# Kernel tuning notes

Hardware: AMD Instinct MI355X
Metric: run time of the kernel (lower is better)

## Reference

```python
import jax, jax.numpy as jnp
import numpy as np

NC, NX, NY = 32, 512, 512
N_LOC = 100000


def setup_inputs() -> dict:
    key = jax.random.key(0)
    k1, k2 = jax.random.split(key)
    x = jax.random.normal(k1, (8, NC, NX, NY), dtype=jnp.float32)
    kernel = jnp.zeros((1, NC, NX, NY), dtype=jnp.float32)
    variable_kernel = jax.random.normal(k2, (N_LOC,), dtype=jnp.float32)
    # unique flat indices into the (NC, NX, NY) kernel volume (cluster locations)
    rng = np.random.default_rng(0)
    loc_idx = jnp.asarray(rng.choice(NC * NX * NY, N_LOC, replace=False).astype(np.int64))
    return {"x": x, "kernel": kernel, "variable_kernel": variable_kernel, "loc_idx": loc_idx}


def fill_kernel(kernel, variable_kernel, loc_idx):
    # scatter ReLU'd trainable values into the sparse PSF locations
    k0 = kernel[0].reshape(-1).at[loc_idx].set(jax.nn.relu(variable_kernel))
    return k0.reshape(NC, NX, NY)


def disperse_all_orders(x, k):
    # per-channel circular convolution with the multi-order dispersion PSF,
    # summed over spectral channels onto the sensor: (b, nx, ny)
    Xf = jnp.fft.rfft2(x, axes=(-2, -1))          # (b, nc, nx, ny//2+1)
    Kf = jnp.fft.rfft2(k, axes=(-2, -1))          # (nc, nx, ny//2+1)
    Yf = jnp.sum(Xf * Kf[None], axis=1)           # (b, nx, ny//2+1)
    return jnp.fft.irfft2(Yf, s=(NX, NY), axes=(-2, -1))


def reference(x, kernel, variable_kernel, loc_idx):
    k = fill_kernel(kernel, variable_kernel, loc_idx)
    return disperse_all_orders(x, k)
```

## Files before the change

kernel.cpp:

```cpp
#include <hip/hip_runtime.h>
#include <cstdint>

#define NXX 512
#define NYY 512
#define NCH 32
#define NB  8
#define NU  257
#define IMG_CPLX (NU*NXX)
#define PIX (NXX*NYY)

__device__ __forceinline__ uint32_t f2bf(float f){
  uint32_t u = __float_as_uint(f);
  return (u + 0x7FFFu + ((u >> 16) & 1u)) >> 16;
}
__device__ __forceinline__ float bf2f(uint32_t h){ return __uint_as_float(h << 16); }
__device__ __forceinline__ uint32_t packbf(float re, float im){ return f2bf(re) | (f2bf(im) << 16); }

#define WAIT_LGKM() asm volatile("s_waitcnt lgkmcnt(0)" ::: "memory")

__device__ __forceinline__ void cmul(float& zr, float& zi, float wr, float wi){
  float r = zr*wr - zi*wi;
  zi = zr*wi + zi*wr;
  zr = r;
}

template<int DIR>
__device__ __forceinline__ void bfly8(float* xr, float* xi){
  const float S = 0.70710678118654752440f;
  float er0=xr[0]+xr[4], ei0=xi[0]+xi[4];
  float er1=xr[1]+xr[5], ei1=xi[1]+xi[5];
  float er2=xr[2]+xr[6], ei2=xi[2]+xi[6];
  float er3=xr[3]+xr[7], ei3=xi[3]+xi[7];
  float or0=xr[0]-xr[4], oi0=xi[0]-xi[4];
  float or1=xr[1]-xr[5], oi1=xi[1]-xi[5];
  float or2=xr[2]-xr[6], oi2=xi[2]-xi[6];
  float or3=xr[3]-xr[7], oi3=xi[3]-xi[7];
  float p0r=er0+er2, p0i=ei0+ei2;
  float p1r=er0-er2, p1i=ei0-ei2;
  float q0r=er1+er3, q0i=ei1+ei3;
  float q1r=er1-er3, q1i=ei1-ei3;
  float w4r, w4i;
  if (DIR<0){ w4r=q1i; w4i=-q1r; } else { w4r=-q1i; w4i=q1r; }
  xr[0]=p0r+q0r; xi[0]=p0i+q0i;
  xr[4]=p0r-q0r; xi[4]=p0i-q0i;
  xr[2]=p1r+w4r; xi[2]=p1i+w4i;
  xr[6]=p1r-w4r; xi[6]=p1i-w4i;
  float f1r,f1i,f2r,f2i,f3r,f3i;
  if (DIR<0){
    f1r=S*(or1+oi1); f1i=S*(oi1-or1);
    f2r=oi2;         f2i=-or2;
    f3r=S*(oi3-or3); f3i=-S*(or3+oi3);
  } else {
    f1r=S*(or1-oi1);  f1i=S*(or1+oi1);
    f2r=-oi2;         f2i=or2;
    f3r=-S*(or3+oi3); f3i=S*(or3-oi3);
  }
  float g0r=or0+f2r, g0i=oi0+f2i;
  float g1r=or0-f2r, g1i=oi0-f2i;
  float h0r=f1r+f3r, h0i=f1i+f3i;
  float h1r=f1r-f3r, h1i=f1i-f3i;
  float v4r, v4i;
  if (DIR<0){ v4r=h1i; v4i=-h1r; } else { v4r=-h1i; v4i=h1r; }
  xr[1]=g0r+h0r; xi[1]=g0i+h0i;
  xr[5]=g0r-h0r; xi[5]=g0i-h0i;
  xr[3]=g1r+v4r; xi[3]=g1i+v4i;
  xr[7]=g1r-v4r; xi[7]=g1i-v4i;
}

__device__ __forceinline__ void make_tw(int t, float* t1r, float* t1i, float* t2r, float* t2i){
  const float TP = 6.283185307179586476925f;
  float s, c;
  sincosf(-TP * (float)t * (1.0f/512.0f), &s, &c);
  t1r[0]=1.0f; t1i[0]=0.0f;
  #pragma unroll
  for (int k=1;k<8;k++){ t1r[k]=t1r[k-1]*c - t1i[k-1]*s; t1i[k]=t1r[k-1]*s + t1i[k-1]*c; }
  sincosf(-TP * (float)(t>>3) * (1.0f/64.0f), &s, &c);
  t2r[0]=1.0f; t2i[0]=0.0f;
  #pragma unroll
  for (int k=1;k<8;k++){ t2r[k]=t2r[k-1]*c - t2i[k-1]*s; t2i[k]=t2r[k-1]*s + t2i[k-1]*c; }
}

template<int DIR>
__device__ __forceinline__ void fft512(float* ar, float* ai, float* sre, float* sim, int t,
    const float* t1r, const float* t1i, const float* t2r, const float* t2i){
  bfly8<DIR>(ar, ai);
  #pragma unroll
  for (int k=1;k<8;k++){ cmul(ar[k], ai[k], t1r[k], (DIR<0)? t1i[k] : -t1i[k]); }
  #pragma unroll
  for (int k=0;k<8;k++){ int d = 8*t + k; d += (d>>5); sre[d]=ar[k]; sim[d]=ai[k]; }
  WAIT_LGKM();
  #pragma unroll
  for (int j=0;j<8;j++){ int s2 = t + (j<<6); s2 += (s2>>5); ar[j]=sre[s2]; ai[j]=sim[s2]; }
  WAIT_LGKM();
  bfly8<DIR>(ar, ai);
  #pragma unroll
  for (int k=1;k<8;k++){ cmul(ar[k], ai[k], t2r[k], (DIR<0)? t2i[k] : -t2i[k]); }
  #pragma unroll
  for (int k=0;k<8;k++){ int d = (t&7) + ((t>>3)<<6) + (k<<3); d += (d>>5); sre[d]=ar[k]; sim[d]=ai[k]; }
  WAIT_LGKM();
  #pragma unroll
  for (int j=0;j<8;j++){ int s2 = t + (j<<6); s2 += (s2>>5); ar[j]=sre[s2]; ai[j]=sim[s2]; }
  WAIT_LGKM();
  bfly8<DIR>(ar, ai);
}

__global__ __launch_bounds__(256) void k_zero(uint4* __restrict__ p, int n4){
  int stride = gridDim.x * 256;
  for (int i = blockIdx.x*256 + threadIdx.x; i < n4; i += stride)
    p[i] = make_uint4(0u,0u,0u,0u);
}

__global__ void k_scatter(const float* __restrict__ vk, const int* __restrict__ loc,
                          float* __restrict__ kbuf, int n){
  int i = blockIdx.x*256 + threadIdx.x;
  if (i < n){ float v = vk[i]; kbuf[loc[i]] = v > 0.0f ? v : 0.0f; }
}

__global__ __launch_bounds__(512) void k_p1(const float* __restrict__ src,
                                            uint32_t* __restrict__ dst){
  __shared__ float sre[8][528], sim[8][528];
  __shared__ uint32_t staged[NU*33];
  const int tid = threadIdx.x;
  const int w = tid >> 6, t = tid & 63;
  const int img = blockIdx.x >> 4;
  const int rblock = (blockIdx.x & 15) << 5;
  float t1r[8],t1i[8],t2r[8],t2i[8];
  make_tw(t, t1r,t1i,t2r,t2i);
  #pragma unroll
  for (int p=0; p<2; p++){
    const int il = (w<<2) + (p<<1);
    const float* rowA = src + (size_t)img*PIX + (size_t)(rblock + il)*NYY;
    float ar[8], ai[8];
    #pragma unroll
    for (int j=0;j<8;j++){ ar[j]=rowA[t+(j<<6)]; ai[j]=rowA[NYY + t + (j<<6)]; }
    fft512<-1>(ar,ai,sre[w],sim[w],t,t1r,t1i,t2r,t2i);
    #pragma unroll
    for (int k=0;k<8;k++){ int d = t+(k<<6); d += (d>>5); sre[w][d]=ar[k]; sim[w][d]=ai[k]; }
    WAIT_LGKM();
    #pragma unroll
    for (int k=0;k<5;k++){
      int u = t + (k<<6);
      if (u < NU){
        int e2 = (512 - u) & 511;
        int du = u + (u>>5), d2 = e2 + (e2>>5);
        float zur=sre[w][du], zui=sim[w][du];
        float zvr=sre[w][d2], zvi=sim[w][d2];
        float Ar=0.5f*(zur+zvr), Ai=0.5f*(zui-zvi);
        float Br=0.5f*(zui+zvi), Bi=0.5f*(zvr-zur);
        staged[u*33 + il]     = packbf(Ar,Ai);
        staged[u*33 + il + 1] = packbf(Br,Bi);
      }
    }
    WAIT_LGKM();
  }
  __syncthreads();
  uint32_t* ob = dst + (size_t)img*IMG_CPLX;
  for (int e = tid; e < NU*32; e += 512){
    int u = e >> 5, il2 = e & 31;
    ob[(size_t)u*NXX + rblock + il2] = staged[u*33 + il2];
  }
}

__global__ __launch_bounds__(512) void k_p2k(uint32_t* __restrict__ rtk){
  __shared__ float sre[8][528], sim[8][528];
  const int w = threadIdx.x >> 6, t = threadIdx.x & 63;
  const int fid = blockIdx.x*8 + w;
  const int c = fid / NU, u = fid % NU;
  float t1r[8],t1i[8],t2r[8],t2i[8];
  make_tw(t, t1r,t1i,t2r,t2i);
  uint32_t* col = rtk + (size_t)c*IMG_CPLX + (size_t)u*NXX;
  float ar[8], ai[8];
  #pragma unroll
  for (int j=0;j<8;j++){ uint32_t v = col[t+(j<<6)]; ar[j]=bf2f(v & 0xFFFFu); ai[j]=bf2f(v >> 16); }
  fft512<-1>(ar,ai,sre[w],sim[w],t,t1r,t1i,t2r,t2i);
  #pragma unroll
  for (int k=0;k<8;k++){ col[t+(k<<6)] = packbf(ar[k], ai[k]); }
}

__global__ __launch_bounds__(512) void k_p3(const uint32_t* __restrict__ rtx,
    const uint32_t* __restrict__ rtk, uint32_t* __restrict__ y3, int b0, int gsh){
  __shared__ float sre[8][528], sim[8][528];
  __shared__ float redr[8][512], redi[8][512];
  const int tid = threadIdx.x;
  const int w = tid >> 6, t = tid & 63;
  const int u  = blockIdx.x >> gsh;
  const int bl = blockIdx.x & ((1<<gsh)-1);
  float t1r[8],t1i[8],t2r[8],t2i[8];
  make_tw(t, t1r,t1i,t2r,t2i);
  float accr[8], acci[8];
  #pragma unroll
  for (int k=0;k<8;k++){ accr[k]=0.0f; acci[k]=0.0f; }
  #pragma unroll
  for (int cc=0; cc<4; cc++){
    const int c = (w<<2) + cc;
    const uint32_t* xc = rtx + ((size_t)(bl*NCH + c))*IMG_CPLX + (size_t)u*NXX;
    const uint32_t* kc = rtk + (size_t)c*IMG_CPLX + (size_t)u*NXX;
    uint32_t xv[8], kv[8];
    #pragma unroll
    for (int j=0;j<8;j++){ xv[j]=xc[t+(j<<6)]; kv[j]=kc[t+(j<<6)]; }
    float ar[8], ai[8];
    #pragma unroll
    for (int j=0;j<8;j++){ ar[j]=bf2f(xv[j] & 0xFFFFu); ai[j]=bf2f(xv[j] >> 16); }
    fft512<-1>(ar,ai,sre[w],sim[w],t,t1r,t1i,t2r,t2i);
    #pragma unroll
    for (int k=0;k<8;k++){
      float kr=bf2f(kv[k] & 0xFFFFu), ki=bf2f(kv[k] >> 16);
      accr[k] += ar[k]*kr - ai[k]*ki;
      acci[k] += ar[k]*ki + ai[k]*kr;
    }
  }
  #pragma unroll
  for (int k=0;k<8;k++){ redr[w][t+(k<<6)] = accr[k]; redi[w][t+(k<<6)] = acci[k]; }
  __syncthreads();
  const float sc = 1.0f/262144.0f;
  float sr=0.0f, si=0.0f;
  #pragma unroll
  for (int ww=0; ww<8; ww++){ sr += redr[ww][tid]; si += redi[ww][tid]; }
  redr[0][tid] = sr*sc; redi[0][tid] = si*sc;
  __syncthreads();
  if (w==0){
    float ar[8], ai[8];
    #pragma unroll
    for (int j=0;j<8;j++){ ar[j]=redr[0][t+(j<<6)]; ai[j]=redi[0][t+(j<<6)]; }
    fft512<1>(ar,ai,sre[0],sim[0],t,t1r,t1i,t2r,t2i);
    uint32_t* yc = y3 + ((size_t)(b0+bl)*NU + u)*NXX;
    #pragma unroll
    for (int k=0;k<8;k++){ yc[t+(k<<6)] = packbf(ar[k], ai[k]); }
  }
}

__global__ __launch_bounds__(512) void k_p4(const uint32_t* __restrict__ y3,
                                            float* __restrict__ out){
  __shared__ float sre[8][528], sim[8][528];
  __shared__ uint32_t sta[NU*17];
  const int tid = threadIdx.x, w = tid>>6, t = tid&63;
  const int b = blockIdx.x >> 5;
  const int i0 = (blockIdx.x & 31) << 4;
  const uint32_t* yb = y3 + (size_t)b*IMG_CPLX;
  for (int e = tid; e < NU*16; e += 512){
    int u = e >> 4, il = e & 15;
    sta[u*17 + il] = yb[(size_t)u*NXX + i0 + il];
  }
  __syncthreads();
  float t1r[8],t1i[8],t2r[8],t2i[8];
  make_tw(t, t1r,t1i,t2r,t2i);
  float ar[8], ai[8];
  #pragma unroll
  for (int j=0;j<8;j++){
    int e = t + (j<<6);
    if (e <= 256){
      uint32_t pa_ = sta[e*17 + 2*w], pb_ = sta[e*17 + 2*w + 1];
      float Ar=bf2f(pa_&0xFFFFu), Ai=bf2f(pa_>>16);
      float Br=bf2f(pb_&0xFFFFu), Bi=bf2f(pb_>>16);
      ar[j] = Ar - Bi; ai[j] = Ai + Br;
    } else {
      int ep = 512 - e;
      uint32_t pa_ = sta[ep*17 + 2*w], pb_ = sta[ep*17 + 2*w + 1];
      float Ar=bf2f(pa_&0xFFFFu), Ai=bf2f(pa_>>16);
      float Br=bf2f(pb_&0xFFFFu), Bi=bf2f(pb_>>16);
      ar[j] = Ar + Bi; ai[j] = Br - Ai;
    }
  }
  fft512<1>(ar,ai,sre[w],sim[w],t,t1r,t1i,t2r,t2i);
  float* ob = out + (size_t)b*PIX + (size_t)(i0 + 2*w)*NYY;
  #pragma unroll
  for (int k=0;k<8;k++){ int n = t+(k<<6); ob[n]=ar[k]; ob[NYY+n]=ai[k]; }
}

extern "C" void kernel_launch(void* const* d_in, const int* in_sizes, int n_in,
                              void* d_out, int out_size, void* d_ws, size_t ws_size,
                              hipStream_t stream) {
  const float* x  = (const float*)d_in[0];
  const float* vk = (const float*)d_in[2];
  const int*   loc= (const int*)d_in[3];
  float* out = (float*)d_out;
  char* ws = (char*)d_ws;
  const int n_loc = in_sizes[2];

  const size_t kbytes   = (size_t)NCH*PIX*4;
  const size_t imgbytes = (size_t)IMG_CPLX*4;

  float*    kbuf = (float*)ws;
  uint32_t* y3   = (uint32_t*)ws;
  uint32_t* rtk  = (uint32_t*)(ws + kbytes);
  uint32_t* rtx  = rtk + (size_t)NCH*IMG_CPLX;

  int G = 8;
  while (G > 1 && kbytes + (size_t)(NCH + NCH*G)*imgbytes > ws_size) G >>= 1;
  const int gsh = (G==8)?3:((G==4)?2:((G==2)?1:0));

  k_zero<<<2048, 256, 0, stream>>>((uint4*)kbuf, (int)(kbytes/16));
  k_scatter<<<(n_loc+255)/256, 256, 0, stream>>>(vk, loc, kbuf, n_loc);
  k_p1<<<NCH*16, 512, 0, stream>>>(kbuf, rtk);
  k_p2k<<<(NCH*NU)/8, 512, 0, stream>>>(rtk);
  for (int b0 = 0; b0 < NB; b0 += G){
    k_p1<<<G*NCH*16, 512, 0, stream>>>(x + (size_t)b0*NCH*PIX, rtx);
    k_p3<<<NU<<gsh, 512, 0, stream>>>(rtx, rtk, y3, b0, gsh);
  }
  k_p4<<<NB*32, 512, 0, stream>>>(y3, out);
}
```

Measured before the change: 193.0 us.

## Store PSF volume as bf16 and vectorize global loads via LDS staging

The scattered PSF buffer becomes bf16 instead of fp32, which halves the zero-fill and the first-pass read traffic for the kernel volume. Row and column loads in the forward FFT passes switch from strided scalar loads to 128-bit vector loads, staged through shared memory and transposed to the per-thread layout. This adds extra LDS round-trips and waits per column, and quantizes the PSF values to bf16 before the FFT.

```diff
diff --git a/kernel.cpp b/kernel.cpp
--- a/kernel.cpp
+++ b/kernel.cpp
@@ -104,6 +104,23 @@
   bfly8<DIR>(ar, ai);
 }
 
+__device__ __forceinline__ void stage_col_bf16(const uint32_t* __restrict__ col, float* S, int t,
+                                               float* ar, float* ai){
+  const uint4* c4 = (const uint4*)col;
+  uint4 a = c4[t], b = c4[64+t];
+  uint32_t wa[4]={a.x,a.y,a.z,a.w}, wb[4]={b.x,b.y,b.z,b.w};
+  #pragma unroll
+  for (int q=0;q<4;q++){
+    int e=4*t+q,   d =e +(e >>5);  S[d ]=__uint_as_float(wa[q]);
+    int e2=e+256,  d2=e2+(e2>>5);  S[d2]=__uint_as_float(wb[q]);
+  }
+  WAIT_LGKM();
+  #pragma unroll
+  for (int j=0;j<8;j++){ int s2=t+(j<<6); s2+=(s2>>5);
+    uint32_t v=__float_as_uint(S[s2]); ar[j]=bf2f(v&0xFFFFu); ai[j]=bf2f(v>>16); }
+  WAIT_LGKM();
+}
+
 __global__ __launch_bounds__(256) void k_zero(uint4* __restrict__ p, int n4){
   int stride = gridDim.x * 256;
   for (int i = blockIdx.x*256 + threadIdx.x; i < n4; i += stride)
@@ -111,12 +128,13 @@
 }
 
 __global__ void k_scatter(const float* __restrict__ vk, const int* __restrict__ loc,
-                          float* __restrict__ kbuf, int n){
+                          uint16_t* __restrict__ kbuf, int n){
   int i = blockIdx.x*256 + threadIdx.x;
-  if (i < n){ float v = vk[i]; kbuf[loc[i]] = v > 0.0f ? v : 0.0f; }
-}
-
-__global__ __launch_bounds__(512) void k_p1(const float* __restrict__ src,
+  if (i < n){ float v = vk[i]; v = v > 0.0f ? v : 0.0f; kbuf[loc[i]] = (uint16_t)f2bf(v); }
+}
+
+template<int BF16>
+__global__ __launch_bounds__(512) void k_p1(const void* __restrict__ srcv,
                                             uint32_t* __restrict__ dst){
   __shared__ float sre[8][528], sim[8][528];
   __shared__ uint32_t staged[NU*33];
@@ -126,16 +144,42 @@
   const int rblock = (blockIdx.x & 15) << 5;
   float t1r[8],t1i[8],t2r[8],t2i[8];
   make_tw(t, t1r,t1i,t2r,t2i);
+  float* S = sre[w];
+  float* T = sim[w];
   #pragma unroll
   for (int p=0; p<2; p++){
     const int il = (w<<2) + (p<<1);
-    const float* rowA = src + (size_t)img*PIX + (size_t)(rblock + il)*NYY;
     float ar[8], ai[8];
-    #pragma unroll
-    for (int j=0;j<8;j++){ ar[j]=rowA[t+(j<<6)]; ai[j]=rowA[NYY + t + (j<<6)]; }
-    fft512<-1>(ar,ai,sre[w],sim[w],t,t1r,t1i,t2r,t2i);
-    #pragma unroll
-    for (int k=0;k<8;k++){ int d = t+(k<<6); d += (d>>5); sre[w][d]=ar[k]; sim[w][d]=ai[k]; }
+    if (BF16){
+      const uint16_t* base = (const uint16_t*)srcv + (size_t)img*PIX + (size_t)(rblock + il)*NYY;
+      const uint4* A4 = (const uint4*)base;
+      uint4 a = A4[t], b = A4[64+t];
+      uint32_t wa[4]={a.x,a.y,a.z,a.w}, wb[4]={b.x,b.y,b.z,b.w};
+      #pragma unroll
+      for (int q=0;q<4;q++){
+        int e0=8*t+2*q, e1=e0+1;
+        int d0=e0+(e0>>5), d1=e1+(e1>>5);
+        S[d0]=bf2f(wa[q]&0xFFFFu); S[d1]=bf2f(wa[q]>>16);
+        T[d0]=bf2f(wb[q]&0xFFFFu); T[d1]=bf2f(wb[q]>>16);
+      }
+      WAIT_LGKM();
+      #pragma unroll
+      for (int j=0;j<8;j++){ int s2=t+(j<<6); s2+=(s2>>5); ar[j]=S[s2]; ai[j]=T[s2]; }
+      WAIT_LGKM();
+    } else {
+      const float* rowA = (const float*)srcv + (size_t)img*PIX + (size_t)(rblock + il)*NYY;
+      const float4* A4 = (const float4*)rowA;
+      float4 a0=A4[t], a1=A4[64+t], b0=A4[128+t], b1=A4[192+t];
+      ((float4*)S)[t]=a0; ((float4*)S)[64+t]=a1;
+      ((float4*)T)[t]=b0; ((float4*)T)[64+t]=b1;
+      WAIT_LGKM();
+      #pragma unroll
+      for (int j=0;j<8;j++){ ar[j]=S[t+(j<<6)]; ai[j]=T[t+(j<<6)]; }
+      WAIT_LGKM();
+    }
+    fft512<-1>(ar,ai,S,T,t,t1r,t1i,t2r,t2i);
+    #pragma unroll
+    for (int k=0;k<8;k++){ int d = t+(k<<6); d += (d>>5); S[d]=ar[k]; T[d]=ai[k]; }
     WAIT_LGKM();
     #pragma unroll
     for (int k=0;k<5;k++){
@@ -143,8 +187,8 @@
       if (u < NU){
         int e2 = (512 - u) & 511;
         int du = u + (u>>5), d2 = e2 + (e2>>5);
-        float zur=sre[w][du], zui=sim[w][du];
-        float zvr=sre[w][d2], zvi=sim[w][d2];
+        float zur=S[du], zui=T[du];
+        float zvr=S[d2], zvi=T[d2];
         float Ar=0.5f*(zur+zvr), Ai=0.5f*(zui-zvi);
         float Br=0.5f*(zui+zvi), Bi=0.5f*(zvr-zur);
         staged[u*33 + il]     = packbf(Ar,Ai);
@@ -170,8 +214,7 @@
   make_tw(t, t1r,t1i,t2r,t2i);
   uint32_t* col = rtk + (size_t)c*IMG_CPLX + (size_t)u*NXX;
   float ar[8], ai[8];
-  #pragma unroll
-  for (int j=0;j<8;j++){ uint32_t v = col[t+(j<<6)]; ar[j]=bf2f(v & 0xFFFFu); ai[j]=bf2f(v >> 16); }
+  stage_col_bf16(col, sre[w], t, ar, ai);
   fft512<-1>(ar,ai,sre[w],sim[w],t,t1r,t1i,t2r,t2i);
   #pragma unroll
   for (int k=0;k<8;k++){ col[t+(k<<6)] = packbf(ar[k], ai[k]); }
@@ -195,12 +238,11 @@
     const int c = (w<<2) + cc;
     const uint32_t* xc = rtx + ((size_t)(bl*NCH + c))*IMG_CPLX + (size_t)u*NXX;
     const uint32_t* kc = rtk + (size_t)c*IMG_CPLX + (size_t)u*NXX;
-    uint32_t xv[8], kv[8];
-    #pragma unroll
-    for (int j=0;j<8;j++){ xv[j]=xc[t+(j<<6)]; kv[j]=kc[t+(j<<6)]; }
+    uint32_t kv[8];
+    #pragma unroll
+    for (int j=0;j<8;j++){ kv[j]=kc[t+(j<<6)]; }
     float ar[8], ai[8];
-    #pragma unroll
-    for (int j=0;j<8;j++){ ar[j]=bf2f(xv[j] & 0xFFFFu); ai[j]=bf2f(xv[j] >> 16); }
+    stage_col_bf16(xc, sre[w], t, ar, ai);
     fft512<-1>(ar,ai,sre[w],sim[w],t,t1r,t1i,t2r,t2i);
     #pragma unroll
     for (int k=0;k<8;k++){
@@ -277,24 +319,24 @@
   char* ws = (char*)d_ws;
   const int n_loc = in_sizes[2];
 
-  const size_t kbytes   = (size_t)NCH*PIX*4;
+  const size_t kbytes16 = (size_t)NCH*PIX*2;
   const size_t imgbytes = (size_t)IMG_CPLX*4;
 
-  float*    kbuf = (float*)ws;
+  uint16_t* kbuf = (uint16_t*)ws;
   uint32_t* y3   = (uint32_t*)ws;
-  uint32_t* rtk  = (uint32_t*)(ws + kbytes);
+  uint32_t* rtk  = (uint32_t*)(ws + kbytes16);
   uint32_t* rtx  = rtk + (size_t)NCH*IMG_CPLX;
 
   int G = 8;
-  while (G > 1 && kbytes + (size_t)(NCH + NCH*G)*imgbytes > ws_size) G >>= 1;
+  while (G > 1 && kbytes16 + (size_t)(NCH + NCH*G)*imgbytes > ws_size) G >>= 1;
   const int gsh = (G==8)?3:((G==4)?2:((G==2)?1:0));
 
-  k_zero<<<2048, 256, 0, stream>>>((uint4*)kbuf, (int)(kbytes/16));
+  k_zero<<<2048, 256, 0, stream>>>((uint4*)kbuf, (int)(kbytes16/16));
   k_scatter<<<(n_loc+255)/256, 256, 0, stream>>>(vk, loc, kbuf, n_loc);
-  k_p1<<<NCH*16, 512, 0, stream>>>(kbuf, rtk);
+  k_p1<1><<<NCH*16, 512, 0, stream>>>(kbuf, rtk);
   k_p2k<<<(NCH*NU)/8, 512, 0, stream>>>(rtk);
   for (int b0 = 0; b0 < NB; b0 += G){
-    k_p1<<<G*NCH*16, 512, 0, stream>>>(x + (size_t)b0*NCH*PIX, rtx);
+    k_p1<0><<<G*NCH*16, 512, 0, stream>>>(x + (size_t)b0*NCH*PIX, rtx);
     k_p3<<<NU<<gsh, 512, 0, stream>>>(rtx, rtk, y3, b0, gsh);
   }
   k_p4<<<NB*32, 512, 0, stream>>>(y3, out);
```

Result: no change. 196.5 us (+1.8%).
